# Kernel optimization log

Measured on AMD Instinct MI355X. Metric: run time of the kernel, lower is better.

The kernel has to match this reference:

```python
import jax, jax.numpy as jnp
import numpy as np

M = 2  # sqrt(n_heads)

def setup_inputs() -> dict:
    key = jax.random.key(0)
    k1, k2, k3 = jax.random.split(key, 3)
    b, H, W, c = 8, 256, 256, 64
    x = jax.random.normal(k1, (b, H, W, c), dtype=jnp.float32)
    # 1x1 conv weights expressed as matrices: qkv [c, 3c], project [c, c]
    scale = 1.0 / np.sqrt(c)
    Wqkv = jax.random.normal(k2, (c, 3 * c), dtype=jnp.float32) * scale
    Wproj = jax.random.normal(k3, (c, c), dtype=jnp.float32) * scale
    return {"x": x, "Wqkv": Wqkv, "Wproj": Wproj}


def reference(x, Wqkv, Wproj):
    b, H, W, c = x.shape
    h, w = H // M, W // M
    temp = c ** (-0.5)  # n_features ** -0.5
    # 1x1 conv qkv projection (bias-free)
    qkv = jnp.einsum('byxc,cd->byxd', x, Wqkv)  # [b,H,W,3c]
    q, k, v = jnp.split(qkv, 3, axis=-1)

    def blk(t):
        # 'b (h m1) (w m2) c -> b (m1 m2) c (h w)'
        t = t.reshape(b, h, M, w, M, c)
        t = t.transpose(0, 2, 4, 5, 1, 3)  # b m1 m2 c h w
        return t.reshape(b, M * M, c, h * w)

    q, k, v = blk(q), blk(k), blk(v)
    # channel-attention: c x c score per block, contracted over hw
    score = jnp.einsum('bncl,bndl->bncd', q, k) * temp
    weight = jax.nn.softmax(score, axis=-1)
    out = jnp.einsum('bncd,bndl->bncl', weight, v)
    # inverse rearrange: 'b (m1 m2) c (h w) -> b (h m1) (w m2) c'
    out = out.reshape(b, M, M, c, h, w).transpose(0, 4, 1, 5, 2, 3).reshape(b, H, W, c)
    # 1x1 conv output projection
    return jnp.einsum('byxc,cd->byxd', out, Wproj)
```

## Files before the change

### kernel.cpp

```cpp
#include <hip/hip_runtime.h>

typedef float f32x4 __attribute__((ext_vector_type(4)));
typedef __bf16 bf16x8 __attribute__((ext_vector_type(8)));
typedef short s16x8 __attribute__((ext_vector_type(8)));

__device__ __forceinline__ unsigned short f2bf(float f) {
  unsigned u = __builtin_bit_cast(unsigned, f);
  return (unsigned short)((u + 0x7fffu + ((u >> 16) & 1u)) >> 16);
}
__device__ __forceinline__ float bf2f(unsigned short s) {
  unsigned u = ((unsigned)s) << 16;
  return __builtin_bit_cast(float, u);
}

#define LSTR 40

__global__ __launch_bounds__(256) void gram_kernel(const float* __restrict__ x,
                                                   float* __restrict__ Gpart,
                                                   int shift, int steps) {
  __shared__ __align__(16) unsigned short xsh[2][64 * LSTR];
  __shared__ __align__(16) unsigned short xsl[2][64 * LSTR];
  const int tid = threadIdx.x;
  const int lane = tid & 63;
  const int wave = tid >> 6;
  const int blk = blockIdx.x;
  const int nchm1 = (1 << shift) - 1;
  const int chunk = blk & nchm1;
  const int bn = blk >> shift;
  const int b = bn >> 2;
  const int m1 = (bn >> 1) & 1;
  const int m2 = bn & 1;
  const int px0 = (tid & 15) * 2;
  const int c0 = (tid >> 4) * 4;
  const int mrow = lane & 15;
  const int k8 = (lane >> 4) * 8;
  const int tr0 = (wave >> 1) * 2;
  const int tc0 = (wave & 1) * 2;

  f32x4 acc[2][2];
#pragma unroll
  for (int i = 0; i < 2; ++i)
#pragma unroll
    for (int j = 0; j < 2; ++j) acc[i][j] = (f32x4){0.f, 0.f, 0.f, 0.f};

  const int l0base = chunk * steps * 32 + px0;
  auto addr = [&](int ks) {
    int l0 = l0base + ks * 32;
    int hy = l0 >> 7, wx = l0 & 127;
    int y = 2 * hy + m1, xx = 2 * wx + m2;
    return x + ((b * 256 + y) * 256 + xx) * 64 + c0;
  };

  const float* p0 = addr(0);
  f32x4 v0 = *(const f32x4*)p0;
  f32x4 v1 = *(const f32x4*)(p0 + 128);
  int pb = 0;

  for (int ks = 0; ks < steps; ++ks) {
#pragma unroll
    for (int i = 0; i < 4; ++i) {
      unsigned short h0 = f2bf(v0[i]), h1 = f2bf(v1[i]);
      unsigned short g0 = f2bf(v0[i] - bf2f(h0)), g1 = f2bf(v1[i] - bf2f(h1));
      *(unsigned*)&xsh[pb][(c0 + i) * LSTR + px0] = (unsigned)h0 | ((unsigned)h1 << 16);
      *(unsigned*)&xsl[pb][(c0 + i) * LSTR + px0] = (unsigned)g0 | ((unsigned)g1 << 16);
    }
    __syncthreads();
    if (ks + 1 < steps) {
      const float* pn = addr(ks + 1);
      v0 = *(const f32x4*)pn;
      v1 = *(const f32x4*)(pn + 128);
    }
    s16x8 rh[2], rl[2], qh[2], ql[2];
#pragma unroll
    for (int i = 0; i < 2; ++i) {
      rh[i] = *(const s16x8*)&xsh[pb][(16 * (tr0 + i) + mrow) * LSTR + k8];
      rl[i] = *(const s16x8*)&xsl[pb][(16 * (tr0 + i) + mrow) * LSTR + k8];
      qh[i] = *(const s16x8*)&xsh[pb][(16 * (tc0 + i) + mrow) * LSTR + k8];
      ql[i] = *(const s16x8*)&xsl[pb][(16 * (tc0 + i) + mrow) * LSTR + k8];
    }
#pragma unroll
    for (int i = 0; i < 2; ++i)
#pragma unroll
      for (int j = 0; j < 2; ++j) {
        bf16x8 ah = __builtin_bit_cast(bf16x8, rh[i]);
        bf16x8 al = __builtin_bit_cast(bf16x8, rl[i]);
        bf16x8 bh = __builtin_bit_cast(bf16x8, qh[j]);
        bf16x8 bl = __builtin_bit_cast(bf16x8, ql[j]);
        acc[i][j] = __builtin_amdgcn_mfma_f32_16x16x32_bf16(ah, bh, acc[i][j], 0, 0, 0);
        acc[i][j] = __builtin_amdgcn_mfma_f32_16x16x32_bf16(ah, bl, acc[i][j], 0, 0, 0);
        acc[i][j] = __builtin_amdgcn_mfma_f32_16x16x32_bf16(al, bh, acc[i][j], 0, 0, 0);
      }
    pb ^= 1;
  }
  float* Gp = Gpart + (((size_t)bn << shift) + chunk) * 4096;
#pragma unroll
  for (int i = 0; i < 2; ++i)
#pragma unroll
    for (int j = 0; j < 2; ++j)
#pragma unroll
      for (int r = 0; r < 4; ++r) {
        int row = 16 * (tr0 + i) + (lane >> 4) * 4 + r;
        int col = 16 * (tc0 + j) + (lane & 15);
        Gp[row * 64 + col] = acc[i][j][r];
      }
}

__device__ __forceinline__ void mm_colA(const float* Ab, const float* Bb,
                                        float* Dst, float scale, int ti4, int tj4) {
  float acc[4][4] = {};
#pragma unroll 8
  for (int kk = 0; kk < 64; ++kk) {
    f32x4 a = *(const f32x4*)&Ab[kk * 68 + ti4];
    f32x4 b = *(const f32x4*)&Bb[kk * 68 + tj4];
#pragma unroll
    for (int i = 0; i < 4; ++i)
#pragma unroll
      for (int j = 0; j < 4; ++j) acc[i][j] += a[i] * b[j];
  }
#pragma unroll
  for (int i = 0; i < 4; ++i) {
    f32x4 o = {acc[i][0] * scale, acc[i][1] * scale, acc[i][2] * scale, acc[i][3] * scale};
    *(f32x4*)&Dst[(ti4 + i) * 68 + tj4] = o;
  }
}

__device__ __forceinline__ void mm_rowA(const float* Ab, const float* Bb,
                                        float* Dst, int ti4, int tj4) {
  float acc[4][4] = {};
#pragma unroll 2
  for (int kk0 = 0; kk0 < 64; kk0 += 4) {
    f32x4 a4[4], b4[4];
#pragma unroll
    for (int i = 0; i < 4; ++i) a4[i] = *(const f32x4*)&Ab[(ti4 + i) * 68 + kk0];
#pragma unroll
    for (int kx = 0; kx < 4; ++kx) b4[kx] = *(const f32x4*)&Bb[(kk0 + kx) * 68 + tj4];
#pragma unroll
    for (int kx = 0; kx < 4; ++kx)
#pragma unroll
      for (int i = 0; i < 4; ++i)
#pragma unroll
        for (int j = 0; j < 4; ++j) acc[i][j] += a4[i][kx] * b4[kx][j];
  }
#pragma unroll
  for (int i = 0; i < 4; ++i) {
    f32x4 o = {acc[i][0], acc[i][1], acc[i][2], acc[i][3]};
    *(f32x4*)&Dst[(ti4 + i) * 64 + tj4] = o;
  }
}

__device__ __forceinline__ void loadW(float* Bsh, const float* W, int ldw, int off, int tid) {
  for (int i = tid * 4; i < 4096; i += 1024) {
    int r = i >> 6, c = i & 63;
    *(f32x4*)&Bsh[r * 68 + c] = *(const f32x4*)&W[r * ldw + off + c];
  }
}

__global__ __launch_bounds__(256) void fuse_kernel(const float* __restrict__ Gpart,
                                                   const float* __restrict__ Wqkv,
                                                   const float* __restrict__ Wproj,
                                                   float* __restrict__ F, int nch) {
  __shared__ __align__(16) float A[64 * 68];
  __shared__ __align__(16) float B[64 * 68];
  __shared__ __align__(16) float T[64 * 68];
  const int tid = threadIdx.x;
  const int bn = blockIdx.x;
  const int ti4 = (tid >> 4) * 4, tj4 = (tid & 15) * 4;

  {
    const float* gp = Gpart + (size_t)bn * nch * 4096;
    for (int i = tid * 4; i < 4096; i += 1024) {
      f32x4 s = {0.f, 0.f, 0.f, 0.f};
      for (int p = 0; p < nch; ++p) s += *(const f32x4*)&gp[p * 4096 + i];
      int r = i >> 6, c = i & 63;
      *(f32x4*)&A[r * 68 + c] = s;
      *(f32x4*)&B[r * 68 + c] = *(const f32x4*)&Wqkv[r * 192 + 64 + c];
    }
  }
  __syncthreads();
  mm_colA(A, B, T, 1.f, ti4, tj4);
  __syncthreads();
  loadW(B, Wqkv, 192, 0, tid);
  __syncthreads();
  mm_colA(B, T, A, 0.125f, ti4, tj4);
  __syncthreads();
  {
    const int row = tid >> 2, q = tid & 3;
    float* Ar = A + row * 68 + q * 16;
    f32x4 v[4];
#pragma unroll
    for (int t = 0; t < 4; ++t) v[t] = *(const f32x4*)&Ar[t * 4];
    float mx = -1e30f;
#pragma unroll
    for (int t = 0; t < 4; ++t)
#pragma unroll
      for (int e = 0; e < 4; ++e) mx = fmaxf(mx, v[t][e]);
    mx = fmaxf(mx, __shfl_xor(mx, 1));
    mx = fmaxf(mx, __shfl_xor(mx, 2));
    float s = 0.f;
#pragma unroll
    for (int t = 0; t < 4; ++t)
#pragma unroll
      for (int e = 0; e < 4; ++e) {
        float ev = __expf(v[t][e] - mx);
        v[t][e] = ev;
        s += ev;
      }
    s += __shfl_xor(s, 1);
    s += __shfl_xor(s, 2);
    float inv = 1.f / s;
#pragma unroll
    for (int t = 0; t < 4; ++t) {
      v[t] *= inv;
      *(f32x4*)&Ar[t * 4] = v[t];
    }
  }
  __syncthreads();
  loadW(B, Wproj, 64, 0, tid);
  __syncthreads();
  mm_colA(A, B, T, 1.f, ti4, tj4);
  __syncthreads();
  loadW(B, Wqkv, 192, 128, tid);
  __syncthreads();
  mm_rowA(B, T, F + bn * 4096, ti4, tj4);
}

__global__ __launch_bounds__(256) void out_kernel(const float* __restrict__ x,
                                                  const float* __restrict__ F,
                                                  float* __restrict__ out) {
  const int tid = threadIdx.x;
  const int lane = tid & 63;
  const int wave = tid >> 6;
  const int blk = blockIdx.x;
  const int hyg = blk & 63;
  const int bn = blk >> 6;
  const int b = bn >> 2;
  const int m1 = (bn >> 1) & 1;
  const int m2 = bn & 1;

  s16x8 bh[2][4], bl[2][4];
  const float* Fp = F + bn * 4096;
#pragma unroll
  for (int ksj = 0; ksj < 2; ++ksj)
#pragma unroll
    for (int tc = 0; tc < 4; ++tc) {
      s16x8 hv, lv;
#pragma unroll
      for (int j = 0; j < 8; ++j) {
        int k = ksj * 32 + (lane >> 4) * 8 + j;
        int e = tc * 16 + (lane & 15);
        float f = Fp[k * 64 + e];
        unsigned short hb = f2bf(f);
        hv[j] = (short)hb;
        lv[j] = (short)f2bf(f - bf2f(hb));
      }
      bh[ksj][tc] = hv;
      bl[ksj][tc] = lv;
    }

  for (int r = 0; r < 2; ++r) {
    int hy = hyg * 2 + r;
    int y = 2 * hy + m1;
    const float* xrow = x + ((b * 256 + y) * 256) * 64;
    float* orow = out + ((b * 256 + y) * 256) * 64;
#pragma unroll
    for (int ptI = 0; ptI < 2; ++ptI) {
      int pt = wave + ptI * 4;
      int wx = pt * 16 + (lane & 15);
      int xx = 2 * wx + m2;
      const float* pp = xrow + xx * 64 + (lane >> 4) * 8;
      s16x8 ah[2], al[2];
#pragma unroll
      for (int ksj = 0; ksj < 2; ++ksj) {
        f32x4 u0 = *(const f32x4*)(pp + ksj * 32);
        f32x4 u1 = *(const f32x4*)(pp + ksj * 32 + 4);
        s16x8 hv, lv;
#pragma unroll
        for (int j = 0; j < 4; ++j) {
          unsigned short hb0 = f2bf(u0[j]);
          unsigned short hb1 = f2bf(u1[j]);
          hv[j] = (short)hb0;
          hv[4 + j] = (short)hb1;
          lv[j] = (short)f2bf(u0[j] - bf2f(hb0));
          lv[4 + j] = (short)f2bf(u1[j] - bf2f(hb1));
        }
        ah[ksj] = hv;
        al[ksj] = lv;
      }
      f32x4 acc[4];
#pragma unroll
      for (int tc = 0; tc < 4; ++tc) acc[tc] = (f32x4){0.f, 0.f, 0.f, 0.f};
#pragma unroll
      for (int ksj = 0; ksj < 2; ++ksj)
#pragma unroll
        for (int tc = 0; tc < 4; ++tc) {
          bf16x8 A_h = __builtin_bit_cast(bf16x8, ah[ksj]);
          bf16x8 A_l = __builtin_bit_cast(bf16x8, al[ksj]);
          bf16x8 B_h = __builtin_bit_cast(bf16x8, bh[ksj][tc]);
          bf16x8 B_l = __builtin_bit_cast(bf16x8, bl[ksj][tc]);
          acc[tc] = __builtin_amdgcn_mfma_f32_16x16x32_bf16(A_h, B_h, acc[tc], 0, 0, 0);
          acc[tc] = __builtin_amdgcn_mfma_f32_16x16x32_bf16(A_h, B_l, acc[tc], 0, 0, 0);
          acc[tc] = __builtin_amdgcn_mfma_f32_16x16x32_bf16(A_l, B_h, acc[tc], 0, 0, 0);
        }
#pragma unroll
      for (int tc = 0; tc < 4; ++tc)
#pragma unroll
        for (int j = 0; j < 4; ++j) {
          int prow = (lane >> 4) * 4 + j;
          int xx2 = 2 * (pt * 16 + prow) + m2;
          __builtin_nontemporal_store(acc[tc][j], &orow[xx2 * 64 + tc * 16 + (lane & 15)]);
        }
    }
  }
}

extern "C" void kernel_launch(void* const* d_in, const int* in_sizes, int n_in,
                              void* d_out, int out_size, void* d_ws, size_t ws_size,
                              hipStream_t stream) {
  (void)in_sizes; (void)n_in; (void)out_size;
  const float* x = (const float*)d_in[0];
  const float* Wqkv = (const float*)d_in[1];
  const float* Wproj = (const float*)d_in[2];
  float* out = (float*)d_out;

  int shift = 5;
  while (shift > 0) {
    size_t need = ((32ull << shift) + 32ull) * 4096ull * 4ull;
    if (need <= ws_size) break;
    --shift;
  }
  const int nch = 1 << shift;
  const int steps = 512 >> shift;

  float* Gpart = (float*)d_ws;
  float* F = Gpart + ((size_t)32 << shift) * 4096;

  gram_kernel<<<32 * nch, 256, 0, stream>>>(x, Gpart, shift, steps);
  fuse_kernel<<<32, 256, 0, stream>>>(Gpart, Wqkv, Wproj, F, nch);
  out_kernel<<<2048, 256, 0, stream>>>(x, F, out);
}
```

Baseline: 309.3 us.

## Split Gram reduction into its own kernel and vectorize Gram and output stores

Moves the sum over partial Gram chunks out of the 32-block fuse kernel into a separate 128-block reduce kernel, so more blocks share that serial reduction. The Gram kernel now writes each accumulator tile as one f32x4 store in transposed order, which is valid because each block's Gram matrix is symmetric. In the output kernel the MFMA operands are swapped so each lane holds four consecutive channels of one pixel, replacing scalar nontemporal stores with f32x4 stores. This adds one kernel launch and a workspace buffer for the reduced Gram matrices.

New measurement: 288.6 us. 1.07x faster.

```diff
diff --git a/kernel.cpp b/kernel.cpp
--- a/kernel.cpp
+++ b/kernel.cpp
@@ -93,16 +93,28 @@
     pb ^= 1;
   }
   float* Gp = Gpart + (((size_t)bn << shift) + chunk) * 4096;
+  const int rowb = (lane >> 4) * 4;
 #pragma unroll
   for (int i = 0; i < 2; ++i)
 #pragma unroll
-    for (int j = 0; j < 2; ++j)
-#pragma unroll
-      for (int r = 0; r < 4; ++r) {
-        int row = 16 * (tr0 + i) + (lane >> 4) * 4 + r;
-        int col = 16 * (tc0 + j) + (lane & 15);
-        Gp[row * 64 + col] = acc[i][j][r];
-      }
+    for (int j = 0; j < 2; ++j) {
+      int col = 16 * (tc0 + j) + (lane & 15);
+      int row0 = 16 * (tr0 + i) + rowb;
+      *(f32x4*)&Gp[col * 64 + row0] = acc[i][j];
+    }
+}
+
+__global__ __launch_bounds__(256) void reduce_kernel(const float* __restrict__ Gpart,
+                                                     float* __restrict__ G, int nch) {
+  const int gid = blockIdx.x * 256 + threadIdx.x;
+  const int i4 = gid * 4;
+  const int bn = i4 >> 12;
+  const int idx = i4 & 4095;
+  const float* gp = Gpart + ((size_t)bn * nch) * 4096 + idx;
+  f32x4 s = {0.f, 0.f, 0.f, 0.f};
+#pragma unroll 8
+  for (int p = 0; p < nch; ++p) s += *(const f32x4*)&gp[(size_t)p * 4096];
+  *(f32x4*)&G[i4] = s;
 }
 
 __device__ __forceinline__ void mm_colA(const float* Ab, const float* Bb,
@@ -155,10 +167,10 @@
   }
 }
 
-__global__ __launch_bounds__(256) void fuse_kernel(const float* __restrict__ Gpart,
+__global__ __launch_bounds__(256) void fuse_kernel(const float* __restrict__ G,
                                                    const float* __restrict__ Wqkv,
                                                    const float* __restrict__ Wproj,
-                                                   float* __restrict__ F, int nch) {
+                                                   float* __restrict__ F) {
   __shared__ __align__(16) float A[64 * 68];
   __shared__ __align__(16) float B[64 * 68];
   __shared__ __align__(16) float T[64 * 68];
@@ -166,15 +178,10 @@
   const int bn = blockIdx.x;
   const int ti4 = (tid >> 4) * 4, tj4 = (tid & 15) * 4;
 
-  {
-    const float* gp = Gpart + (size_t)bn * nch * 4096;
-    for (int i = tid * 4; i < 4096; i += 1024) {
-      f32x4 s = {0.f, 0.f, 0.f, 0.f};
-      for (int p = 0; p < nch; ++p) s += *(const f32x4*)&gp[p * 4096 + i];
-      int r = i >> 6, c = i & 63;
-      *(f32x4*)&A[r * 68 + c] = s;
-      *(f32x4*)&B[r * 68 + c] = *(const f32x4*)&Wqkv[r * 192 + 64 + c];
-    }
+  for (int i = tid * 4; i < 4096; i += 1024) {
+    int r = i >> 6, c = i & 63;
+    *(f32x4*)&A[r * 68 + c] = *(const f32x4*)&G[bn * 4096 + i];
+    *(f32x4*)&B[r * 68 + c] = *(const f32x4*)&Wqkv[r * 192 + 64 + c];
   }
   __syncthreads();
   mm_colA(A, B, T, 1.f, ti4, tj4);
@@ -257,6 +264,8 @@
       bl[ksj][tc] = lv;
     }
 
+  const int e4 = (lane >> 4) * 4;
+
   for (int r = 0; r < 2; ++r) {
     int hy = hyg * 2 + r;
     int y = 2 * hy + m1;
@@ -297,18 +306,15 @@
           bf16x8 A_l = __builtin_bit_cast(bf16x8, al[ksj]);
           bf16x8 B_h = __builtin_bit_cast(bf16x8, bh[ksj][tc]);
           bf16x8 B_l = __builtin_bit_cast(bf16x8, bl[ksj][tc]);
-          acc[tc] = __builtin_amdgcn_mfma_f32_16x16x32_bf16(A_h, B_h, acc[tc], 0, 0, 0);
-          acc[tc] = __builtin_amdgcn_mfma_f32_16x16x32_bf16(A_h, B_l, acc[tc], 0, 0, 0);
-          acc[tc] = __builtin_amdgcn_mfma_f32_16x16x32_bf16(A_l, B_h, acc[tc], 0, 0, 0);
+          acc[tc] = __builtin_amdgcn_mfma_f32_16x16x32_bf16(B_h, A_h, acc[tc], 0, 0, 0);
+          acc[tc] = __builtin_amdgcn_mfma_f32_16x16x32_bf16(B_l, A_h, acc[tc], 0, 0, 0);
+          acc[tc] = __builtin_amdgcn_mfma_f32_16x16x32_bf16(B_h, A_l, acc[tc], 0, 0, 0);
         }
-#pragma unroll
-      for (int tc = 0; tc < 4; ++tc)
-#pragma unroll
-        for (int j = 0; j < 4; ++j) {
-          int prow = (lane >> 4) * 4 + j;
-          int xx2 = 2 * (pt * 16 + prow) + m2;
-          __builtin_nontemporal_store(acc[tc][j], &orow[xx2 * 64 + tc * 16 + (lane & 15)]);
-        }
+      float* op = orow + xx * 64;
+#pragma unroll
+      for (int tc = 0; tc < 4; ++tc) {
+        __builtin_nontemporal_store(acc[tc], (f32x4*)&op[tc * 16 + e4]);
+      }
     }
   }
 }
@@ -324,7 +330,7 @@
 
   int shift = 5;
   while (shift > 0) {
-    size_t need = ((32ull << shift) + 32ull) * 4096ull * 4ull;
+    size_t need = ((32ull << shift) + 64ull) * 4096ull * 4ull;
     if (need <= ws_size) break;
     --shift;
   }
@@ -332,9 +338,11 @@
   const int steps = 512 >> shift;
 
   float* Gpart = (float*)d_ws;
-  float* F = Gpart + ((size_t)32 << shift) * 4096;
+  float* G = Gpart + ((size_t)32 << shift) * 4096;
+  float* F = G + 32 * 4096;
 
   gram_kernel<<<32 * nch, 256, 0, stream>>>(x, Gpart, shift, steps);
-  fuse_kernel<<<32, 256, 0, stream>>>(Gpart, Wqkv, Wproj, F, nch);
+  reduce_kernel<<<128, 256, 0, stream>>>(Gpart, G, nch);
+  fuse_kernel<<<32, 256, 0, stream>>>(G, Wqkv, Wproj, F);
   out_kernel<<<2048, 256, 0, stream>>>(x, F, out);
 }
```
